# Kernel optimization log

Measured on AMD Instinct MI355X. Metric: run time of the kernel, lower is better.

## Reference

```python
import jax, jax.numpy as jnp
import numpy as np

B, T, D_BERT, D_LSTM, N_CLASS, X = 32, 512, 768, 256, 16, 10
H2 = D_LSTM // 2  # per-direction hidden size


def setup_inputs() -> dict:
    key = jax.random.key(0)
    ks = jax.random.split(key, 24)
    rn = lambda k, s: jax.random.normal(k, s, jnp.float32) * 0.05
    return {
        "x": jax.random.normal(ks[0], (B, T, D_BERT), jnp.float32),
        "mask": jnp.ones((B, T), jnp.int32),
        # encoder BiLSTM (PyTorch gate order i,f,g,o)
        "Wih_f": rn(ks[1], (4 * H2, D_BERT)), "Whh_f": rn(ks[2], (4 * H2, H2)),
        "bih_f": rn(ks[3], (4 * H2,)), "bhh_f": rn(ks[4], (4 * H2,)),
        "Wih_r": rn(ks[5], (4 * H2, D_BERT)), "Whh_r": rn(ks[6], (4 * H2, H2)),
        "bih_r": rn(ks[7], (4 * H2,)), "bhh_r": rn(ks[8], (4 * H2,)),
        # attention projections
        "fc1_w": rn(ks[9], (X, 2 * D_LSTM)),
        "fc2_w": rn(ks[10], (1, X)),
        "fc3_w": rn(ks[11], (D_LSTM, 2 * D_LSTM)), "fc3_b": rn(ks[12], (D_LSTM,)),
        # decoder LSTMCell + output linear
        "Wih_d": rn(ks[13], (4 * D_LSTM, D_LSTM + N_CLASS)),
        "Whh_d": rn(ks[14], (4 * D_LSTM, D_LSTM)),
        "bih_d": rn(ks[15], (4 * D_LSTM,)), "bhh_d": rn(ks[16], (4 * D_LSTM,)),
        "lin_w": rn(ks[17], (N_CLASS, D_LSTM)), "lin_b": rn(ks[18], (N_CLASS,)),
    }


def _cell(xt, h, c, Wih, Whh, bih, bhh):
    g = xt @ Wih.T + bih + h @ Whh.T + bhh
    i, f, gg, o = jnp.split(g, 4, axis=-1)
    c = jax.nn.sigmoid(f) * c + jax.nn.sigmoid(i) * jnp.tanh(gg)
    h = jax.nn.sigmoid(o) * jnp.tanh(c)
    return h, c


def _lstm(x_tbd, Wih, Whh, bih, bhh):
    # x_tbd: [T, B, D] -> hs [T, B, H]
    Bn, H = x_tbd.shape[1], Whh.shape[1]
    def step(carry, xt):
        h, c = _cell(xt, carry[0], carry[1], Wih, Whh, bih, bhh)
        return (h, c), h
    z = jnp.zeros((Bn, H), x_tbd.dtype)
    _, hs = jax.lax.scan(step, (z, z), x_tbd)
    return hs


def _forward(x, mask, Wih_f, Whh_f, bih_f, bhh_f, Wih_r, Whh_r, bih_r, bhh_r,
             fc1_w, fc2_w, fc3_w, fc3_b, Wih_d, Whh_d, bih_d, bhh_d, lin_w, lin_b):
    xt = x.transpose(1, 0, 2)  # [T,B,D_BERT]
    hf = _lstm(xt, Wih_f, Whh_f, bih_f, bhh_f)
    hr = _lstm(xt[::-1], Wih_r, Whh_r, bih_r, bhh_r)[::-1]
    hs = jnp.concatenate([hf, hr], -1).transpose(1, 0, 2)  # [B,T,D_LSTM]

    # additive attention: fc1(cat(query,key)) == query@Wq.T + key@Wk.T
    Wq, Wk = fc1_w[:, :D_LSTM], fc1_w[:, D_LSTM:]
    qp = hs @ Wq.T  # [B,T,X]
    kp = hs @ Wk.T  # [B,T,X]
    a = jnp.tanh(qp[:, :, None, :] + kp[:, None, :, :]) @ fc2_w[0]  # [B,T,T]
    m = jnp.where(mask == 0, -jnp.inf, 0.0)[:, None, :]  # [B,1,T]
    w = jax.nn.softmax(a + m, axis=-1)
    ctx = jnp.einsum('bij,bjd->bid', w, hs)  # [B,T,D_LSTM]
    y_enc = jnp.concatenate([hs, ctx], -1) @ fc3_w.T + fc3_b  # [B,T,D_LSTM]

    init_h = hs[:, -1, :]
    def dstep(carry, xt_):
        h, c, y = carry
        h, c = _cell(jnp.concatenate([xt_, y], -1), h, c, Wih_d, Whh_d, bih_d, bhh_d)
        y = jax.nn.softmax(h @ lin_w.T + lin_b, axis=-1)
        return (h, c, y), y
    init = (init_h, jnp.zeros_like(init_h), jnp.zeros((x.shape[0], N_CLASS), x.dtype))
    _, ys = jax.lax.scan(dstep, init, y_enc.transpose(1, 0, 2))
    return ys.transpose(1, 0, 2)  # [B,T,N_CLASS]


def reference(x, mask, Wih_f, Whh_f, bih_f, bhh_f, Wih_r, Whh_r, bih_r, bhh_r,
              fc1_w, fc2_w, fc3_w, fc3_b, Wih_d, Whh_d, bih_d, bhh_d, lin_w, lin_b):
    return _forward(x, mask, Wih_f, Whh_f, bih_f, bhh_f, Wih_r, Whh_r, bih_r, bhh_r,
                    fc1_w, fc2_w, fc3_w, fc3_b, Wih_d, Whh_d, bih_d, bhh_d, lin_w, lin_b)
```

## Files before the change

### kernel.cpp

```cpp
#include <hip/hip_runtime.h>

#define TSEQ 512
#define NB   32
#define DB   768
#define H2E  128
#define DL   256
#define NC   16

typedef unsigned long long ull;
typedef float f32x4 __attribute__((ext_vector_type(4)));
typedef short bf16x8 __attribute__((ext_vector_type(8)));
typedef unsigned short u16x8 __attribute__((ext_vector_type(8)));

__device__ __forceinline__ float sigf(float x) { return 1.0f / (1.0f + __expf(-x)); }
__device__ __forceinline__ float tanhfast(float x) { return 1.0f - 2.0f / (1.0f + __expf(2.0f * x)); }

__device__ __forceinline__ void cvt_split(float a, unsigned short& hi, unsigned short& lo) {
    unsigned u = __float_as_uint(a);
    unsigned h = (u + 0x7FFFu + ((u >> 16) & 1u)) >> 16;
    float hf = __uint_as_float(h << 16);
    float d = a - hf;
    unsigned ud = __float_as_uint(d);
    unsigned l = (ud + 0x7FFFu + ((ud >> 16) & 1u)) >> 16;
    hi = (unsigned short)h;
    lo = (unsigned short)l;
}

#define LDST 40
template <int MODE>
__global__ __launch_bounds__(256) void gemm_mfma(
    const float* __restrict__ A, int lda,
    const float* __restrict__ W, int ldw,
    const float* __restrict__ b1, const float* __restrict__ b2,
    float* __restrict__ C, int ldc, int K)
{
    __shared__ unsigned short Ah[128][LDST];
    __shared__ unsigned short Al[128][LDST];
    __shared__ unsigned short Wh[128][LDST];
    __shared__ unsigned short Wl[128][LDST];

    const int tid = threadIdx.x;
    const int m0 = blockIdx.x * 128;
    const int n0 = blockIdx.y * 128;
    const int wave = tid >> 6, lane = tid & 63;
    const int wr = wave >> 1, wc = wave & 1;
    const int fr = lane & 15;
    const int fq = lane >> 4;
    const int srow = tid >> 1, skoff = (tid & 1) * 16;

    f32x4 acc[4][4] = {};

    for (int k0 = 0; k0 < K; k0 += 32) {
        __syncthreads();
        {
            const float* src = A + (size_t)(m0 + srow) * lda + k0 + skoff;
            u16x8 vh0, vh1, vl0, vl1;
#pragma unroll
            for (int e = 0; e < 8; ++e) {
                unsigned short h, l;
                cvt_split(src[e], h, l);
                vh0[e] = h; vl0[e] = l;
                cvt_split(src[e + 8], h, l);
                vh1[e] = h; vl1[e] = l;
            }
            *(u16x8*)&Ah[srow][skoff]     = vh0;
            *(u16x8*)&Ah[srow][skoff + 8] = vh1;
            *(u16x8*)&Al[srow][skoff]     = vl0;
            *(u16x8*)&Al[srow][skoff + 8] = vl1;
        }
        {
            const float* src = W + (size_t)(n0 + srow) * ldw + k0 + skoff;
            u16x8 vh0, vh1, vl0, vl1;
#pragma unroll
            for (int e = 0; e < 8; ++e) {
                unsigned short h, l;
                cvt_split(src[e], h, l);
                vh0[e] = h; vl0[e] = l;
                cvt_split(src[e + 8], h, l);
                vh1[e] = h; vl1[e] = l;
            }
            *(u16x8*)&Wh[srow][skoff]     = vh0;
            *(u16x8*)&Wh[srow][skoff + 8] = vh1;
            *(u16x8*)&Wl[srow][skoff]     = vl0;
            *(u16x8*)&Wl[srow][skoff + 8] = vl1;
        }
        __syncthreads();

        bf16x8 ah[4], al[4], bh[4], bl[4];
#pragma unroll
        for (int i = 0; i < 4; ++i) {
            const int r = wr * 64 + i * 16 + fr;
            ah[i] = *(const bf16x8*)&Ah[r][fq * 8];
            al[i] = *(const bf16x8*)&Al[r][fq * 8];
        }
#pragma unroll
        for (int j = 0; j < 4; ++j) {
            const int r = wc * 64 + j * 16 + fr;
            bh[j] = *(const bf16x8*)&Wh[r][fq * 8];
            bl[j] = *(const bf16x8*)&Wl[r][fq * 8];
        }
#pragma unroll
        for (int i = 0; i < 4; ++i)
#pragma unroll
            for (int j = 0; j < 4; ++j) {
                acc[i][j] = __builtin_amdgcn_mfma_f32_16x16x32_bf16(ah[i], bh[j], acc[i][j], 0, 0, 0);
                acc[i][j] = __builtin_amdgcn_mfma_f32_16x16x32_bf16(ah[i], bl[j], acc[i][j], 0, 0, 0);
                acc[i][j] = __builtin_amdgcn_mfma_f32_16x16x32_bf16(al[i], bh[j], acc[i][j], 0, 0, 0);
            }
    }

#pragma unroll
    for (int i = 0; i < 4; ++i) {
#pragma unroll
        for (int r = 0; r < 4; ++r) {
            int gm = m0 + wr * 64 + i * 16 + fq * 4 + r;
            int orow;
            if (MODE == 0) orow = gm;
            else {
                int bb = gm >> 9;
                int tt = gm & (TSEQ - 1);
                orow = (MODE == 1 ? tt : (TSEQ - 1 - tt)) * NB + bb;
            }
            float* crow = C + (size_t)orow * ldc;
#pragma unroll
            for (int j = 0; j < 4; ++j) {
                int gn = n0 + wc * 64 + j * 16 + fr;
                float bias = (b1 ? b1[gn] : 0.f) + (b2 ? b2[gn] : 0.f);
                crow[gn] = acc[i][j][r] + bias;
            }
        }
    }
}

template <int MODE>
__global__ __launch_bounds__(256) void gemm_nt(
    const float* __restrict__ A, int lda,
    const float* __restrict__ W, int ldw,
    const float* __restrict__ b1, const float* __restrict__ b2,
    float* __restrict__ C, int ldc, int N, int K)
{
    __shared__ float As[16][68];
    __shared__ float Ws[16][68];
    const int tid = threadIdx.x;
    const int m0 = blockIdx.x * 64;
    const int n0 = blockIdx.y * 64;
    const int tx = tid & 15, ty = tid >> 4;
    const int lrow = tid >> 2;
    const int lk = (tid & 3) * 4;
    float acc[4][4] = {};

    for (int k0 = 0; k0 < K; k0 += 16) {
        float4 av = *(const float4*)(A + (size_t)(m0 + lrow) * lda + k0 + lk);
        float4 wv = make_float4(0.f, 0.f, 0.f, 0.f);
        if (n0 + lrow < N)
            wv = *(const float4*)(W + (size_t)(n0 + lrow) * ldw + k0 + lk);
        As[lk + 0][lrow] = av.x; As[lk + 1][lrow] = av.y;
        As[lk + 2][lrow] = av.z; As[lk + 3][lrow] = av.w;
        Ws[lk + 0][lrow] = wv.x; Ws[lk + 1][lrow] = wv.y;
        Ws[lk + 2][lrow] = wv.z; Ws[lk + 3][lrow] = wv.w;
        __syncthreads();
#pragma unroll
        for (int kk = 0; kk < 16; ++kk) {
            float a0 = As[kk][ty * 4 + 0], a1 = As[kk][ty * 4 + 1];
            float a2 = As[kk][ty * 4 + 2], a3 = As[kk][ty * 4 + 3];
            float w0 = Ws[kk][tx * 4 + 0], w1 = Ws[kk][tx * 4 + 1];
            float w2 = Ws[kk][tx * 4 + 2], w3 = Ws[kk][tx * 4 + 3];
            acc[0][0] += a0 * w0; acc[0][1] += a0 * w1; acc[0][2] += a0 * w2; acc[0][3] += a0 * w3;
            acc[1][0] += a1 * w0; acc[1][1] += a1 * w1; acc[1][2] += a1 * w2; acc[1][3] += a1 * w3;
            acc[2][0] += a2 * w0; acc[2][1] += a2 * w1; acc[2][2] += a2 * w2; acc[2][3] += a2 * w3;
            acc[3][0] += a3 * w0; acc[3][1] += a3 * w1; acc[3][2] += a3 * w2; acc[3][3] += a3 * w3;
        }
        __syncthreads();
    }

#pragma unroll
    for (int i = 0; i < 4; ++i) {
        int gm = m0 + ty * 4 + i;
        int orow;
        if (MODE == 0) orow = gm;
        else {
            int bb = gm >> 9;
            int tt = gm & (TSEQ - 1);
            orow = (MODE == 1 ? tt : (TSEQ - 1 - tt)) * NB + bb;
        }
#pragma unroll
        for (int j = 0; j < 4; ++j) {
            int gn = n0 + tx * 4 + j;
            if (gn < N) {
                float bias = (b1 ? b1[gn] : 0.f) + (b2 ? b2[gn] : 0.f);
                C[(size_t)orow * ldc + gn] = acc[i][j] + bias;
            }
        }
    }
}

__global__ __launch_bounds__(512) void enc_scan(
    const float* __restrict__ Gf, const float* __restrict__ Gr,
    const float* __restrict__ Whh_f, const float* __restrict__ Whh_r,
    float* __restrict__ hs_ctx)
{
    const int dir = blockIdx.x & 1;
    const int b = blockIdx.x >> 1;
    const float* __restrict__ G = dir ? Gr : Gf;
    const float* __restrict__ Whh = dir ? Whh_r : Whh_f;
    const int j = threadIdx.x;

    __shared__ float4 h4[H2E / 4];
    __shared__ float gates[4 * H2E];
    float* h_s = (float*)h4;

    float4 w[32];
#pragma unroll
    for (int k = 0; k < 32; ++k)
        w[k] = *(const float4*)(Whh + (size_t)j * H2E + k * 4);

    float c = 0.f;
    if (j < H2E) h_s[j] = 0.f;
    __syncthreads();

    for (int t = 0; t < TSEQ; ++t) {
        const float* grow = G + ((size_t)t * NB + b) * 512;
        float acc = grow[j];
#pragma unroll
        for (int k = 0; k < 32; ++k) {
            float4 hv = h4[k];
            acc += w[k].x * hv.x + w[k].y * hv.y + w[k].z * hv.z + w[k].w * hv.w;
        }
        gates[j] = acc;
        __syncthreads();
        if (j < H2E) {
            float ig = sigf(gates[j]);
            float fg = sigf(gates[j + H2E]);
            float gg = tanhfast(gates[j + 2 * H2E]);
            float og = sigf(gates[j + 3 * H2E]);
            c = fg * c + ig * gg;
            float h = og * tanhfast(c);
            h_s[j] = h;
            int tout = dir ? (TSEQ - 1 - t) : t;
            hs_ctx[((size_t)b * TSEQ + tout) * 512 + dir * H2E + j] = h;
        }
        __syncthreads();
    }
}

__global__ __launch_bounds__(256) void attn_w(
    const float* __restrict__ qp, const float* __restrict__ kp,
    const int* __restrict__ mask, const float* __restrict__ fc2,
    float* __restrict__ wout)
{
    const int bi = blockIdx.x;
    const int b = bi >> 9;
    const int tid = threadIdx.x;
    __shared__ float kps[TSEQ * 11];
    __shared__ float red[8];

    const float* kpb = kp + (size_t)b * TSEQ * 10;
    for (int idx = tid; idx < TSEQ * 10; idx += 256) {
        int j = idx / 10, xx = idx - j * 10;
        kps[j * 11 + xx] = kpb[idx];
    }
    float q[10], vv[10];
#pragma unroll
    for (int xx = 0; xx < 10; ++xx) {
        q[xx] = qp[(size_t)bi * 10 + xx];
        vv[xx] = fc2[xx];
    }
    __syncthreads();

    float a[2];
#pragma unroll
    for (int jj = 0; jj < 2; ++jj) {
        int j = tid + jj * 256;
        float s = 0.f;
#pragma unroll
        for (int xx = 0; xx < 10; ++xx)
            s += vv[xx] * tanhfast(q[xx] + kps[j * 11 + xx]);
        if (mask[(size_t)b * TSEQ + j] == 0) s = -1e30f;
        a[jj] = s;
    }

    float m = fmaxf(a[0], a[1]);
#pragma unroll
    for (int o = 32; o >= 1; o >>= 1) m = fmaxf(m, __shfl_xor(m, o));
    if ((tid & 63) == 0) red[tid >> 6] = m;
    __syncthreads();
    m = fmaxf(fmaxf(red[0], red[1]), fmaxf(red[2], red[3]));

    float e0 = __expf(a[0] - m), e1 = __expf(a[1] - m);
    float s = e0 + e1;
#pragma unroll
    for (int o = 32; o >= 1; o >>= 1) s += __shfl_xor(s, o);
    if ((tid & 63) == 0) red[4 + (tid >> 6)] = s;
    __syncthreads();
    s = (red[4] + red[5]) + (red[6] + red[7]);
    float inv = 1.0f / s;
    wout[(size_t)bi * TSEQ + tid] = e0 * inv;
    wout[(size_t)bi * TSEQ + tid + 256] = e1 * inv;
}

__global__ __launch_bounds__(256) void bgemm_nn(
    const float* __restrict__ Wmat,
    float* __restrict__ hs_ctx)
{
    __shared__ float As[16][68];
    __shared__ float Bs[16][68];
    const int tid = threadIdx.x;
    const int b = blockIdx.z;
    const int i0 = blockIdx.x * 64;
    const int d0 = blockIdx.y * 64;
    const int tx = tid & 15, ty = tid >> 4;
    float acc[4][4] = {};
    const float* Ab = Wmat + (size_t)b * TSEQ * TSEQ;
    const float* Bb = hs_ctx + (size_t)b * TSEQ * 512;

    for (int k0 = 0; k0 < TSEQ; k0 += 16) {
        {
            int r = tid >> 2, kq = (tid & 3) * 4;
            float4 v = *(const float4*)(Ab + (size_t)(i0 + r) * TSEQ + k0 + kq);
            As[kq + 0][r] = v.x; As[kq + 1][r] = v.y; As[kq + 2][r] = v.z; As[kq + 3][r] = v.w;
        }
        {
            int kk = tid >> 4, dq = (tid & 15) * 4;
            float4 v = *(const float4*)(Bb + (size_t)(k0 + kk) * 512 + d0 + dq);
            *(float4*)&Bs[kk][dq] = v;
        }
        __syncthreads();
#pragma unroll
        for (int kk = 0; kk < 16; ++kk) {
            float a0 = As[kk][ty * 4 + 0], a1 = As[kk][ty * 4 + 1];
            float a2 = As[kk][ty * 4 + 2], a3 = As[kk][ty * 4 + 3];
            float b0 = Bs[kk][tx * 4 + 0], b1 = Bs[kk][tx * 4 + 1];
            float b2 = Bs[kk][tx * 4 + 2], b3 = Bs[kk][tx * 4 + 3];
            acc[0][0] += a0 * b0; acc[0][1] += a0 * b1; acc[0][2] += a0 * b2; acc[0][3] += a0 * b3;
            acc[1][0] += a1 * b0; acc[1][1] += a1 * b1; acc[1][2] += a1 * b2; acc[1][3] += a1 * b3;
            acc[2][0] += a2 * b0; acc[2][1] += a2 * b1; acc[2][2] += a2 * b2; acc[2][3] += a2 * b3;
            acc[3][0] += a3 * b0; acc[3][1] += a3 * b1; acc[3][2] += a3 * b2; acc[3][3] += a3 * b3;
        }
        __syncthreads();
    }
#pragma unroll
    for (int i = 0; i < 4; ++i)
#pragma unroll
        for (int j = 0; j < 4; ++j)
            hs_ctx[((size_t)b * TSEQ + i0 + ty * 4 + i) * 512 + 256 + d0 + tx * 4 + j] = acc[i][j];
}

__global__ __launch_bounds__(256) void dec_init5(
    const float* __restrict__ hs_ctx, ull* hbuf)
{
    const int gid = blockIdx.x * 256 + threadIdx.x;
    for (int idx = gid; idx < 16384; idx += 16 * 256) {
        ull v = 0ull;
        if (idx < 8192) {
            int b = idx >> 8, u = idx & 255;
            float hv = hs_ctx[((size_t)b * TSEQ + (TSEQ - 1)) * 512 + u];
            v = (1ull << 32) | (ull)__float_as_uint(hv);
        }
        __hip_atomic_store(hbuf + idx, v, __ATOMIC_RELAXED, __HIP_MEMORY_SCOPE_AGENT);
    }
}

__global__ __launch_bounds__(320) void dec_scan10(
    const float* __restrict__ Gd,
    const float* __restrict__ Whh,
    const float* __restrict__ Wih,
    const float* __restrict__ lin_w,
    const float* __restrict__ lin_b,
    ull* hbuf,
    float* __restrict__ out)
{
    const int tid = threadIdx.x;
    const int rg  = blockIdx.x & 15;
    const int bg  = blockIdx.x >> 4;
    const int wave = tid / 64;
    const int lane = tid & 63;
    const int fr = lane & 15;
    const int fq = lane >> 4;
    const bool isw4 = (wave == 4);
    const int ybb = (lane >> 4) & 3;
    const int ycls = lane & 15;

    __shared__ unsigned short wbh[64][264];
    __shared__ unsigned short wbl[64][264];
    __shared__ unsigned short lwh[16][264];
    __shared__ unsigned short lwl[16][264];
    __shared__ unsigned short hbh[4][264];
    __shared__ unsigned short hbl[4][264];
    __shared__ float gpart[4][4][18];
    __shared__ float lgp[4][18];
    __shared__ float wylds[64][17];

    for (int idx = tid; idx < 64 * 256; idx += 320) {
        int row = idx >> 8, c = idx & 255;
        int j = ((row >> 4) << 8) + rg * 16 + (row & 15);
        unsigned short h, l;
        cvt_split(Whh[(size_t)j * 256 + c], h, l);
        wbh[row][c] = h;
        wbl[row][c] = l;
    }
    for (int idx = tid; idx < 16 * 256; idx += 320) {
        int row = idx >> 8, c = idx & 255;
        unsigned short h, l;
        cvt_split(lin_w[(size_t)row * 256 + c], h, l);
        lwh[row][c] = h;
        lwl[row][c] = l;
    }
    for (int idx = tid; idx < 64 * 16; idx += 320) {
        int r = idx >> 4, c = idx & 15;
        int j = ((r >> 4) << 8) + rg * 16 + (r & 15);
        wylds[r][c] = Wih[(size_t)j * 272 + 256 + c];
    }
    const float lb = lin_b[ycls];
    float cstate = 0.f;
    __syncthreads();

    for (int t = 0; t <= TSEQ; ++t) {
        const unsigned want = (unsigned)(t + 1);
        const ull* hsrc = hbuf + (size_t)(t & 1) * 8192 + (size_t)bg * 1024;

        float gdv[4] = {0.f, 0.f, 0.f, 0.f};
        if (isw4 && t < TSEQ) {
            const float* gb = Gd + ((size_t)t * NB + bg * 4 + ybb) * 1024 + rg * 16 + ycls;
#pragma unroll
            for (int q = 0; q < 4; ++q) gdv[q] = gb[q * 256];
        }
        __builtin_amdgcn_sched_barrier(0);

        if (tid < 256) {
            ull h0, h1, h2, h3;
            for (;;) {
                h0 = __hip_atomic_load(hsrc + tid,       __ATOMIC_RELAXED, __HIP_MEMORY_SCOPE_AGENT);
                h1 = __hip_atomic_load(hsrc + tid + 256, __ATOMIC_RELAXED, __HIP_MEMORY_SCOPE_AGENT);
                h2 = __hip_atomic_load(hsrc + tid + 512, __ATOMIC_RELAXED, __HIP_MEMORY_SCOPE_AGENT);
                h3 = __hip_atomic_load(hsrc + tid + 768, __ATOMIC_RELAXED, __HIP_MEMORY_SCOPE_AGENT);
                if (((unsigned)(h0 >> 32) == want) && ((unsigned)(h1 >> 32) == want) &&
                    ((unsigned)(h2 >> 32) == want) && ((unsigned)(h3 >> 32) == want))
                    break;
                __builtin_amdgcn_s_sleep(1);
            }
            unsigned short hh, hl;
            cvt_split(__uint_as_float((unsigned)h0), hh, hl);
            hbh[0][tid] = hh; hbl[0][tid] = hl;
            cvt_split(__uint_as_float((unsigned)h1), hh, hl);
            hbh[1][tid] = hh; hbl[1][tid] = hl;
            cvt_split(__uint_as_float((unsigned)h2), hh, hl);
            hbh[2][tid] = hh; hbl[2][tid] = hl;
            cvt_split(__uint_as_float((unsigned)h3), hh, hl);
            hbh[3][tid] = hh; hbl[3][tid] = hl;
        }
        __syncthreads();

        {
            f32x4 acc1 = {}, acc2 = {};
            const int abrow = lane & 3;
            const unsigned short* browh = isw4 ? &lwh[fr][0] : &wbh[wave * 16 + fr][0];
            const unsigned short* browl = isw4 ? &lwl[fr][0] : &wbl[wave * 16 + fr][0];
#pragma unroll
            for (int ks = 0; ks < 8; ++ks) {
                const int kc = ks * 32 + fq * 8;
                bf16x8 ahi = *(const bf16x8*)&hbh[abrow][kc];
                bf16x8 alo = *(const bf16x8*)&hbl[abrow][kc];
                bf16x8 bhi = *(const bf16x8*)&browh[kc];
                bf16x8 blo = *(const bf16x8*)&browl[kc];
                acc1 = __builtin_amdgcn_mfma_f32_16x16x32_bf16(ahi, bhi, acc1, 0, 0, 0);
                acc2 = __builtin_amdgcn_mfma_f32_16x16x32_bf16(ahi, blo, acc2, 0, 0, 0);
                acc2 = __builtin_amdgcn_mfma_f32_16x16x32_bf16(alo, bhi, acc2, 0, 0, 0);
            }
            if (fq == 0) {
#pragma unroll
                for (int reg = 0; reg < 4; ++reg) {
                    float v = acc1[reg] + acc2[reg];
                    if (isw4) lgp[reg][fr] = v;
                    else      gpart[wave][reg][fr] = v;
                }
            }
        }
        __syncthreads();

        if (isw4) {
            const int bb = ybb, u = ycls;
            float yv = 0.f;
            if (t > 0) {
                float lv = lgp[bb][u] + lb;
                float m = lv;
#pragma unroll
                for (int o = 1; o < 16; o <<= 1) m = fmaxf(m, __shfl_xor(m, o, 16));
                float e = __expf(lv - m);
                float ss = e;
#pragma unroll
                for (int o = 1; o < 16; o <<= 1) ss += __shfl_xor(ss, o, 16);
                yv = e / ss;
                if (rg == 0)
                    out[(((size_t)(bg * 4 + bb)) * TSEQ + (t - 1)) * NC + u] = yv;
            }
            if (t < TSEQ) {
                float g[4];
#pragma unroll
                for (int q = 0; q < 4; ++q) {
                    float s = gpart[q][bb][u] + gdv[q];
                    const int r = q * 16 + u;
#pragma unroll
                    for (int c = 0; c < 16; ++c) {
                        float yc = __shfl(yv, (lane & 48) | c);
                        s += wylds[r][c] * yc;
                    }
                    g[q] = s;
                }
                float ig = sigf(g[0]), fg = sigf(g[1]);
                float gv = tanhfast(g[2]), og = sigf(g[3]);
                cstate = fg * cstate + ig * gv;
                float h = og * tanhfast(cstate);
                const ull tagbits = ((ull)(unsigned)(t + 2)) << 32;
                const size_t oidx = (size_t)((t + 1) & 1) * 8192
                                  + (size_t)(bg * 4 + bb) * 256 + rg * 16 + u;
                __hip_atomic_store(hbuf + oidx, tagbits | (ull)__float_as_uint(h),
                                   __ATOMIC_RELAXED, __HIP_MEMORY_SCOPE_AGENT);
            }
        }
        if (t == TSEQ) break;
    }
}

extern "C" void kernel_launch(void* const* d_in, const int* in_sizes, int n_in,
                              void* d_out, int out_size, void* d_ws, size_t ws_size,
                              hipStream_t stream)
{
    const float* x     = (const float*)d_in[0];
    const int*   mask  = (const int*)d_in[1];
    const float* Wih_f = (const float*)d_in[2];
    const float* Whh_f = (const float*)d_in[3];
    const float* bih_f = (const float*)d_in[4];
    const float* bhh_f = (const float*)d_in[5];
    const float* Wih_r = (const float*)d_in[6];
    const float* Whh_r = (const float*)d_in[7];
    const float* bih_r = (const float*)d_in[8];
    const float* bhh_r = (const float*)d_in[9];
    const float* fc1_w = (const float*)d_in[10];
    const float* fc2_w = (const float*)d_in[11];
    const float* fc3_w = (const float*)d_in[12];
    const float* fc3_b = (const float*)d_in[13];
    const float* Wih_d = (const float*)d_in[14];
    const float* Whh_d = (const float*)d_in[15];
    const float* bih_d = (const float*)d_in[16];
    const float* bhh_d = (const float*)d_in[17];
    const float* lin_w = (const float*)d_in[18];
    const float* lin_b = (const float*)d_in[19];

    float* ws = (float*)d_ws;
    float* Gf   = ws;
    float* Gr   = ws + 8388608;
    float* hs   = ws + 16777216;
    float* wat  = ws + 25165824;
    float* qp   = ws + 33554432;
    float* kp   = ws + 33718272;
    float* Gd   = ws;
    float* yenc = wat;
    ull* hbuf = (ull*)(wat + 4194304);

    float* outp = (float*)d_out;
    const int M = NB * TSEQ;
    dim3 blk(256);

    gemm_mfma<1><<<dim3(M / 128, 4), blk, 0, stream>>>(x, DB, Wih_f, DB, bih_f, bhh_f, Gf, 512, DB);
    gemm_mfma<2><<<dim3(M / 128, 4), blk, 0, stream>>>(x, DB, Wih_r, DB, bih_r, bhh_r, Gr, 512, DB);
    enc_scan<<<dim3(64), dim3(512), 0, stream>>>(Gf, Gr, Whh_f, Whh_r, hs);
    gemm_nt<0><<<dim3(M / 64, 1), blk, 0, stream>>>(hs, 512, fc1_w, 512, nullptr, nullptr, qp, 10, 10, 256);
    gemm_nt<0><<<dim3(M / 64, 1), blk, 0, stream>>>(hs, 512, fc1_w + 256, 512, nullptr, nullptr, kp, 10, 10, 256);
    attn_w<<<dim3(M), blk, 0, stream>>>(qp, kp, mask, fc2_w, wat);
    bgemm_nn<<<dim3(8, 4, NB), blk, 0, stream>>>(wat, hs);
    gemm_mfma<0><<<dim3(M / 128, 2), blk, 0, stream>>>(hs, 512, fc3_w, 512, fc3_b, nullptr, yenc, 256, 512);
    dec_init5<<<dim3(16), blk, 0, stream>>>(hs, hbuf);
    gemm_mfma<1><<<dim3(M / 128, 8), blk, 0, stream>>>(yenc, 256, Wih_d, 272, bih_d, bhh_d, Gd, 1024, 256);
    dec_scan10<<<dim3(128), dim3(320), 0, stream>>>(Gd, Whh_d, Wih_d, lin_w, lin_b, hbuf, outp);
}
```

Baseline: 2.434 ms.

## Move attention-context batched GEMM to split-bf16 MFMA and pre-split decoder hidden state

Replaces the scalar FP32 attention-context batched GEMM with an MFMA kernel using a 3-term bf16 hi/lo split. A new transpose kernel pre-converts hs into transposed hi/lo bf16 buffers, and the attention weights are split on the fly. Separately, the decoder now publishes its hidden state already split into hi/lo bf16 halves, removing the cvt_split step from the consumer spin path on the critical recurrent loop. The split-bf16 product drops the lo*lo term, which slightly lowers precision, and the transpose kernel is an extra launch.

```diff
diff --git a/kernel.cpp b/kernel.cpp
--- a/kernel.cpp
+++ b/kernel.cpp
@@ -127,6 +127,128 @@
                 int gn = n0 + wc * 64 + j * 16 + fr;
                 float bias = (b1 ? b1[gn] : 0.f) + (b2 ? b2[gn] : 0.f);
                 crow[gn] = acc[i][j][r] + bias;
+            }
+        }
+    }
+}
+
+__global__ __launch_bounds__(256) void hs_transpose(
+    const float* __restrict__ hs,
+    unsigned short* __restrict__ Th, unsigned short* __restrict__ Tl)
+{
+    __shared__ float T[64][65];
+    const int tid = threadIdx.x;
+    const int b  = blockIdx.z;
+    const int j0 = blockIdx.x * 64;
+    const int d0 = blockIdx.y * 64;
+    const float* src = hs + ((size_t)b * TSEQ + j0) * 512 + d0;
+#pragma unroll
+    for (int it = 0; it < 4; ++it) {
+        int jl = it * 16 + (tid >> 4);
+        int dl = (tid & 15) * 4;
+        float4 v = *(const float4*)(src + (size_t)jl * 512 + dl);
+        T[jl][dl] = v.x; T[jl][dl + 1] = v.y; T[jl][dl + 2] = v.z; T[jl][dl + 3] = v.w;
+    }
+    __syncthreads();
+#pragma unroll
+    for (int it = 0; it < 4; ++it) {
+        int dl = it * 16 + (tid >> 4);
+        int jl = (tid & 15) * 4;
+        ushort4 hi4, lo4;
+        unsigned short h, l;
+        cvt_split(T[jl][dl], h, l);     hi4.x = h; lo4.x = l;
+        cvt_split(T[jl + 1][dl], h, l); hi4.y = h; lo4.y = l;
+        cvt_split(T[jl + 2][dl], h, l); hi4.z = h; lo4.z = l;
+        cvt_split(T[jl + 3][dl], h, l); hi4.w = h; lo4.w = l;
+        size_t off = ((size_t)b * 256 + d0 + dl) * 512 + j0 + jl;
+        *(ushort4*)(Th + off) = hi4;
+        *(ushort4*)(Tl + off) = lo4;
+    }
+}
+
+__global__ __launch_bounds__(256) void bgemm_mfma(
+    const float* __restrict__ Wmat,
+    const unsigned short* __restrict__ Th, const unsigned short* __restrict__ Tl,
+    float* __restrict__ hs_ctx)
+{
+    __shared__ unsigned short Ah[128][LDST];
+    __shared__ unsigned short Al[128][LDST];
+    __shared__ unsigned short Bh[128][LDST];
+    __shared__ unsigned short Bl[128][LDST];
+
+    const int tid = threadIdx.x;
+    const int b  = blockIdx.z;
+    const int m0 = blockIdx.x * 128;
+    const int n0 = blockIdx.y * 128;
+    const int wave = tid >> 6, lane = tid & 63;
+    const int wr = wave >> 1, wc = wave & 1;
+    const int fr = lane & 15;
+    const int fq = lane >> 4;
+    const int srow = tid >> 1, skoff = (tid & 1) * 16;
+
+    f32x4 acc[4][4] = {};
+
+    for (int k0 = 0; k0 < TSEQ; k0 += 32) {
+        __syncthreads();
+        {
+            const float* src = Wmat + (size_t)b * TSEQ * TSEQ
+                             + (size_t)(m0 + srow) * TSEQ + k0 + skoff;
+            u16x8 vh0, vh1, vl0, vl1;
+#pragma unroll
+            for (int e = 0; e < 8; ++e) {
+                unsigned short h, l;
+                cvt_split(src[e], h, l);
+                vh0[e] = h; vl0[e] = l;
+                cvt_split(src[e + 8], h, l);
+                vh1[e] = h; vl1[e] = l;
+            }
+            *(u16x8*)&Ah[srow][skoff]     = vh0;
+            *(u16x8*)&Ah[srow][skoff + 8] = vh1;
+            *(u16x8*)&Al[srow][skoff]     = vl0;
+            *(u16x8*)&Al[srow][skoff + 8] = vl1;
+        }
+        {
+            size_t off = ((size_t)b * 256 + n0 + srow) * 512 + k0 + skoff;
+            *(u16x8*)&Bh[srow][skoff]     = *(const u16x8*)(Th + off);
+            *(u16x8*)&Bh[srow][skoff + 8] = *(const u16x8*)(Th + off + 8);
+            *(u16x8*)&Bl[srow][skoff]     = *(const u16x8*)(Tl + off);
+            *(u16x8*)&Bl[srow][skoff + 8] = *(const u16x8*)(Tl + off + 8);
+        }
+        __syncthreads();
+
+        bf16x8 ah[4], al[4], bh[4], bl[4];
+#pragma unroll
+        for (int i = 0; i < 4; ++i) {
+            const int r = wr * 64 + i * 16 + fr;
+            ah[i] = *(const bf16x8*)&Ah[r][fq * 8];
+            al[i] = *(const bf16x8*)&Al[r][fq * 8];
+        }
+#pragma unroll
+        for (int j = 0; j < 4; ++j) {
+            const int r = wc * 64 + j * 16 + fr;
+            bh[j] = *(const bf16x8*)&Bh[r][fq * 8];
+            bl[j] = *(const bf16x8*)&Bl[r][fq * 8];
+        }
+#pragma unroll
+        for (int i = 0; i < 4; ++i)
+#pragma unroll
+            for (int j = 0; j < 4; ++j) {
+                acc[i][j] = __builtin_amdgcn_mfma_f32_16x16x32_bf16(ah[i], bh[j], acc[i][j], 0, 0, 0);
+                acc[i][j] = __builtin_amdgcn_mfma_f32_16x16x32_bf16(ah[i], bl[j], acc[i][j], 0, 0, 0);
+                acc[i][j] = __builtin_amdgcn_mfma_f32_16x16x32_bf16(al[i], bh[j], acc[i][j], 0, 0, 0);
+            }
+    }
+
+#pragma unroll
+    for (int i = 0; i < 4; ++i) {
+#pragma unroll
+        for (int r = 0; r < 4; ++r) {
+            int gm = m0 + wr * 64 + i * 16 + fq * 4 + r;
+            float* crow = hs_ctx + ((size_t)b * TSEQ + gm) * 512 + 256;
+#pragma unroll
+            for (int j = 0; j < 4; ++j) {
+                int gn = n0 + wc * 64 + j * 16 + fr;
+                crow[gn] = acc[i][j][r];
             }
         }
     }
@@ -298,54 +420,7 @@
     wout[(size_t)bi * TSEQ + tid + 256] = e1 * inv;
 }
 
-__global__ __launch_bounds__(256) void bgemm_nn(
-    const float* __restrict__ Wmat,
-    float* __restrict__ hs_ctx)
-{
-    __shared__ float As[16][68];
-    __shared__ float Bs[16][68];
-    const int tid = threadIdx.x;
-    const int b = blockIdx.z;
-    const int i0 = blockIdx.x * 64;
-    const int d0 = blockIdx.y * 64;
-    const int tx = tid & 15, ty = tid >> 4;
-    float acc[4][4] = {};
-    const float* Ab = Wmat + (size_t)b * TSEQ * TSEQ;
-    const float* Bb = hs_ctx + (size_t)b * TSEQ * 512;
-
-    for (int k0 = 0; k0 < TSEQ; k0 += 16) {
-        {
-            int r = tid >> 2, kq = (tid & 3) * 4;
-            float4 v = *(const float4*)(Ab + (size_t)(i0 + r) * TSEQ + k0 + kq);
-            As[kq + 0][r] = v.x; As[kq + 1][r] = v.y; As[kq + 2][r] = v.z; As[kq + 3][r] = v.w;
-        }
-        {
-            int kk = tid >> 4, dq = (tid & 15) * 4;
-            float4 v = *(const float4*)(Bb + (size_t)(k0 + kk) * 512 + d0 + dq);
-            *(float4*)&Bs[kk][dq] = v;
-        }
-        __syncthreads();
-#pragma unroll
-        for (int kk = 0; kk < 16; ++kk) {
-            float a0 = As[kk][ty * 4 + 0], a1 = As[kk][ty * 4 + 1];
-            float a2 = As[kk][ty * 4 + 2], a3 = As[kk][ty * 4 + 3];
-            float b0 = Bs[kk][tx * 4 + 0], b1 = Bs[kk][tx * 4 + 1];
-            float b2 = Bs[kk][tx * 4 + 2], b3 = Bs[kk][tx * 4 + 3];
-            acc[0][0] += a0 * b0; acc[0][1] += a0 * b1; acc[0][2] += a0 * b2; acc[0][3] += a0 * b3;
-            acc[1][0] += a1 * b0; acc[1][1] += a1 * b1; acc[1][2] += a1 * b2; acc[1][3] += a1 * b3;
-            acc[2][0] += a2 * b0; acc[2][1] += a2 * b1; acc[2][2] += a2 * b2; acc[2][3] += a2 * b3;
-            acc[3][0] += a3 * b0; acc[3][1] += a3 * b1; acc[3][2] += a3 * b2; acc[3][3] += a3 * b3;
-        }
-        __syncthreads();
-    }
-#pragma unroll
-    for (int i = 0; i < 4; ++i)
-#pragma unroll
-        for (int j = 0; j < 4; ++j)
-            hs_ctx[((size_t)b * TSEQ + i0 + ty * 4 + i) * 512 + 256 + d0 + tx * 4 + j] = acc[i][j];
-}
-
-__global__ __launch_bounds__(256) void dec_init5(
+__global__ __launch_bounds__(256) void dec_init6(
     const float* __restrict__ hs_ctx, ull* hbuf)
 {
     const int gid = blockIdx.x * 256 + threadIdx.x;
@@ -354,13 +429,15 @@
         if (idx < 8192) {
             int b = idx >> 8, u = idx & 255;
             float hv = hs_ctx[((size_t)b * TSEQ + (TSEQ - 1)) * 512 + u];
-            v = (1ull << 32) | (ull)__float_as_uint(hv);
+            unsigned short hh, hl;
+            cvt_split(hv, hh, hl);
+            v = (1ull << 32) | ((ull)hh << 16) | (ull)hl;
         }
         __hip_atomic_store(hbuf + idx, v, __ATOMIC_RELAXED, __HIP_MEMORY_SCOPE_AGENT);
     }
 }
 
-__global__ __launch_bounds__(320) void dec_scan10(
+__global__ __launch_bounds__(320) void dec_scan11(
     const float* __restrict__ Gd,
     const float* __restrict__ Whh,
     const float* __restrict__ Wih,
@@ -438,15 +515,10 @@
                     break;
                 __builtin_amdgcn_s_sleep(1);
             }
-            unsigned short hh, hl;
-            cvt_split(__uint_as_float((unsigned)h0), hh, hl);
-            hbh[0][tid] = hh; hbl[0][tid] = hl;
-            cvt_split(__uint_as_float((unsigned)h1), hh, hl);
-            hbh[1][tid] = hh; hbl[1][tid] = hl;
-            cvt_split(__uint_as_float((unsigned)h2), hh, hl);
-            hbh[2][tid] = hh; hbl[2][tid] = hl;
-            cvt_split(__uint_as_float((unsigned)h3), hh, hl);
-            hbh[3][tid] = hh; hbl[3][tid] = hl;
+            hbh[0][tid] = (unsigned short)(h0 >> 16); hbl[0][tid] = (unsigned short)h0;
+            hbh[1][tid] = (unsigned short)(h1 >> 16); hbl[1][tid] = (unsigned short)h1;
+            hbh[2][tid] = (unsigned short)(h2 >> 16); hbl[2][tid] = (unsigned short)h2;
+            hbh[3][tid] = (unsigned short)(h3 >> 16); hbl[3][tid] = (unsigned short)h3;
         }
         __syncthreads();
 
@@ -510,10 +582,13 @@
                 float gv = tanhfast(g[2]), og = sigf(g[3]);
                 cstate = fg * cstate + ig * gv;
                 float h = og * tanhfast(cstate);
-                const ull tagbits = ((ull)(unsigned)(t + 2)) << 32;
+                unsigned short hh, hl;
+                cvt_split(h, hh, hl);
+                const ull word = (((ull)(unsigned)(t + 2)) << 32)
+                               | ((ull)hh << 16) | (ull)hl;
                 const size_t oidx = (size_t)((t + 1) & 1) * 8192
                                   + (size_t)(bg * 4 + bb) * 256 + rg * 16 + u;
-                __hip_atomic_store(hbuf + oidx, tagbits | (ull)__float_as_uint(h),
+                __hip_atomic_store(hbuf + oidx, word,
                                    __ATOMIC_RELAXED, __HIP_MEMORY_SCOPE_AGENT);
             }
         }
@@ -556,6 +631,8 @@
     float* Gd   = ws;
     float* yenc = wat;
     ull* hbuf = (ull*)(wat + 4194304);
+    unsigned short* hsT_hi = (unsigned short*)ws;
+    unsigned short* hsT_lo = (unsigned short*)(ws + 2097152);
 
     float* outp = (float*)d_out;
     const int M = NB * TSEQ;
@@ -564,12 +641,13 @@
     gemm_mfma<1><<<dim3(M / 128, 4), blk, 0, stream>>>(x, DB, Wih_f, DB, bih_f, bhh_f, Gf, 512, DB);
     gemm_mfma<2><<<dim3(M / 128, 4), blk, 0, stream>>>(x, DB, Wih_r, DB, bih_r, bhh_r, Gr, 512, DB);
     enc_scan<<<dim3(64), dim3(512), 0, stream>>>(Gf, Gr, Whh_f, Whh_r, hs);
+    hs_transpose<<<dim3(8, 4, NB), blk, 0, stream>>>(hs, hsT_hi, hsT_lo);
     gemm_nt<0><<<dim3(M / 64, 1), blk, 0, stream>>>(hs, 512, fc1_w, 512, nullptr, nullptr, qp, 10, 10, 256);
     gemm_nt<0><<<dim3(M / 64, 1), blk, 0, stream>>>(hs, 512, fc1_w + 256, 512, nullptr, nullptr, kp, 10, 10, 256);
     attn_w<<<dim3(M), blk, 0, stream>>>(qp, kp, mask, fc2_w, wat);
-    bgemm_nn<<<dim3(8, 4, NB), blk, 0, stream>>>(wat, hs);
+    bgemm_mfma<<<dim3(4, 2, NB), blk, 0, stream>>>(wat, hsT_hi, hsT_lo, hs);
     gemm_mfma<0><<<dim3(M / 128, 2), blk, 0, stream>>>(hs, 512, fc3_w, 512, fc3_b, nullptr, yenc, 256, 512);
-    dec_init5<<<dim3(16), blk, 0, stream>>>(hs, hbuf);
+    dec_init6<<<dim3(16), blk, 0, stream>>>(hs, hbuf);
     gemm_mfma<1><<<dim3(M / 128, 8), blk, 0, stream>>>(yenc, 256, Wih_d, 272, bih_d, bhh_d, Gd, 1024, 256);
-    dec_scan10<<<dim3(128), dim3(320), 0, stream>>>(Gd, Whh_d, Wih_d, lin_w, lin_b, hbuf, outp);
-}
+    dec_scan11<<<dim3(128), dim3(320), 0, stream>>>(Gd, Whh_d, Wih_d, lin_w, lin_b, hbuf, outp);
+}
```

Result: faster. 2.384 ms (median of 2 runs) (-2.1%).
